# Optimization experiments

Hardware: AMD Instinct MI355X
Metric: run time of the kernel (lower is better)

## Reference

```python
import jax, jax.numpy as jnp
import numpy as np

B, M, N, D = 32, 10, 1000, 128
DEMAND_SCALER, SPEED_SCALER, PREF_SCALER = 40.0, 1.0, 1.0


def _pos_encoding(m, d, dtype):
    # standard sinusoidal PE over agent positions 0..m-1
    pos = jnp.arange(m, dtype=dtype)[:, None]
    div = jnp.exp(jnp.arange(0, d, 2, dtype=dtype) * (-jnp.log(jnp.asarray(10000.0, dtype)) / d))
    ang = pos * div  # (m, d/2)
    return jnp.stack([jnp.sin(ang), jnp.cos(ang)], axis=-1).reshape(m, d)  # even=sin, odd=cos


def setup_inputs() -> dict:
    key = jax.random.key(0)
    ks = jax.random.split(key, 14)
    return {
        "locs": jax.random.uniform(ks[0], (B, M + N, 2), jnp.float32),
        "capacity": jax.random.uniform(ks[1], (B, M), jnp.float32),
        "speed": jax.random.uniform(ks[2], (B, M), jnp.float32),
        "demand": jax.random.uniform(ks[3], (B, 1, M + N), jnp.float32),
        "agents_preference": jax.random.uniform(ks[4], (B, M, M + N), jnp.float32),
        "action_mask": jnp.ones((B, M, M + N), dtype=bool),
        "W_depot": jax.random.normal(ks[5], (D, 2), jnp.float32) * 0.1,
        "W_posproj": jax.random.normal(ks[6], (D, D), jnp.float32) * 0.05,
        "alpha": jnp.ones((1,), jnp.float32),
        "W_agents": jax.random.normal(ks[7], (D, 4), jnp.float32) * 0.1,
        "W_depot_agents": jax.random.normal(ks[8], (D, 2 * D), jnp.float32) * 0.05,
        "W_clients": jax.random.normal(ks[9], (D, 5), jnp.float32) * 0.1,
        "W_pref": jax.random.normal(ks[10], (D, 1), jnp.float32) * 0.1,
        "W_final": jax.random.normal(ks[11], (D, 3 * D), jnp.float32) * 0.05,
    }


def reference(locs, capacity, speed, demand, agents_preference, action_mask,
              W_depot, W_posproj, alpha, W_agents, W_depot_agents, W_clients,
              W_pref, W_final):
    m = action_mask.shape[-2]
    d = W_final.shape[0]
    depot_locs = locs[:, :m]            # (B, m, 2)
    agents_locs = locs[:, :m]
    clients_locs = locs[:, m:]          # (B, N, 2)

    # depot branch with positional encoding
    dep_emb = depot_locs @ W_depot.T                                   # (B, m, D)
    pe = _pos_encoding(m, d, dep_emb.dtype)                            # (m, D)
    depot_embedding = dep_emb + alpha[0] * (pe @ W_posproj.T)          # broadcast over B

    # agents branch
    agents_feats = jnp.concatenate(
        [agents_locs, capacity[..., None] / DEMAND_SCALER, speed[..., None] / SPEED_SCALER], axis=-1)
    agents_embedding = agents_feats @ W_agents.T                       # (B, m, D)
    depot_agents_embedding = jnp.concatenate(
        [depot_embedding, agents_embedding], axis=-1) @ W_depot_agents.T  # (B, m, D)

    # clients branch (with polar feats)
    demands = demand[:, 0, m:]                                         # (B, N)
    centered = clients_locs - depot_locs[:, 0:1]                       # (B, N, 2)
    dist = jnp.linalg.norm(centered, axis=-1, keepdims=True)
    angle = jnp.arctan2(centered[..., 1:], centered[..., :1])
    clients_feats = jnp.concatenate(
        [clients_locs, demands[..., None] / DEMAND_SCALER, dist, angle], axis=-1)
    clients_embedding = clients_feats @ W_clients.T                    # (B, N, D)

    nodes_embedding = jnp.concatenate([agents_embedding, clients_embedding], axis=1)  # (B, m+N, D)

    # fused final projection: Linear(3D, D) on cat([nodes, pref_embed, depot_agents])
    # == nodes @ Wn.T  +  pref_embed @ Wp.T  +  depot_agents @ Wd.T, broadcast over dims.
    # pref_embed = pref[..., None] * W_pref[:, 0]  (rank-1), so pref_embed @ Wp.T = pref[..., None] * (Wp @ W_pref[:, 0])
    Wn, Wp, Wd = W_final[:, :d], W_final[:, d:2 * d], W_final[:, 2 * d:]
    v_pref = Wp @ W_pref[:, 0]                                         # (D,)
    pref = agents_preference / PREF_SCALER                             # (B, m, m+N)
    combined_embedding = (
        (nodes_embedding @ Wn.T)[:, None, :, :]                        # (B, 1, m+N, D)
        + pref[..., None] * v_pref                                     # (B, m, m+N, D)
        + (depot_agents_embedding @ Wd.T)[:, :, None, :]               # (B, m, 1, D)
    )
    return nodes_embedding, combined_embedding
```

## Files before the change

kernel.cpp:

```cpp
#include <hip/hip_runtime.h>
#include <math.h>

#define BB 32
#define MM 10
#define NNODES 1010
#define DD 128
#define RPB 16
#define NG 64

__global__ __launch_bounds__(512) void k_front(
    const float* __restrict__ locs,
    const float* __restrict__ capacity,
    const float* __restrict__ speed,
    const float* __restrict__ W_depot,
    const float* __restrict__ W_posproj,
    const float* __restrict__ alpha,
    const float* __restrict__ W_agents,
    const float* __restrict__ W_da,
    const float* __restrict__ W_pref,
    const float* __restrict__ W_final,
    float* __restrict__ out_nodes,
    float* __restrict__ ws_daWd,
    float* __restrict__ ws_wnT,
    float* __restrict__ ws_vpref)
{
    const int bk = blockIdx.x;
    const int t = threadIdx.x;

    if (bk < BB) {
        const int b = bk;
        const int d = t >> 2;
        const int q = t & 3;

        __shared__ float pe_s[MM][DD];
        __shared__ float cat_s[2 * DD];
        __shared__ float da_s[DD];

        for (int idx = t; idx < MM * DD; idx += 512) {
            const int m = idx >> 7;
            const int k = idx & (DD - 1);
            const int i = k >> 1;
            const float div = expf((float)(2 * i) * (-logf(10000.0f) / (float)DD));
            const float ang = (float)m * div;
            pe_s[m][k] = (k & 1) ? cosf(ang) : sinf(ang);
        }

        float4 wpp[8], wfd[8], wda[16];
        {
            const float4* p = (const float4*)(W_posproj + (size_t)d * DD + q * 32);
            #pragma unroll
            for (int i = 0; i < 8; ++i) wpp[i] = p[i];
        }
        {
            const float4* p = (const float4*)(W_da + (size_t)d * 256 + q * 64);
            #pragma unroll
            for (int i = 0; i < 16; ++i) wda[i] = p[i];
        }
        {
            const float4* p = (const float4*)(W_final + (size_t)d * 384 + 256 + q * 32);
            #pragma unroll
            for (int i = 0; i < 8; ++i) wfd[i] = p[i];
        }
        const float wd0 = W_depot[d * 2 + 0], wd1 = W_depot[d * 2 + 1];
        const float wa0 = W_agents[d * 4 + 0], wa1 = W_agents[d * 4 + 1];
        const float wa2 = W_agents[d * 4 + 2], wa3 = W_agents[d * 4 + 3];
        const float al = alpha[0];
        __syncthreads();

        for (int m = 0; m < MM; ++m) {
            float pp = 0.0f;
            {
                const float4* pe4 = (const float4*)(&pe_s[m][q * 32]);
                #pragma unroll
                for (int i = 0; i < 8; ++i) {
                    const float4 w = wpp[i], x = pe4[i];
                    pp = fmaf(w.x, x.x, fmaf(w.y, x.y, fmaf(w.z, x.z, fmaf(w.w, x.w, pp))));
                }
            }
            pp += __shfl_xor(pp, 1, 4);
            pp += __shfl_xor(pp, 2, 4);

            if (q == 0) {
                const float lx = locs[((size_t)b * NNODES + m) * 2 + 0];
                const float ly = locs[((size_t)b * NNODES + m) * 2 + 1];
                const float dep = fmaf(lx, wd0, fmaf(ly, wd1, al * pp));
                const float cap = capacity[b * MM + m] * (1.0f / 40.0f);
                const float spd = speed[b * MM + m];
                const float ag = fmaf(lx, wa0, fmaf(ly, wa1,
                                 fmaf(cap, wa2, spd * wa3)));
                out_nodes[((size_t)b * NNODES + m) * DD + d] = ag;
                cat_s[d] = dep;
                cat_s[DD + d] = ag;
            }
            __syncthreads();

            float da = 0.0f;
            {
                const float4* c4 = (const float4*)(cat_s + q * 64);
                #pragma unroll
                for (int i = 0; i < 16; ++i) {
                    const float4 w = wda[i], x = c4[i];
                    da = fmaf(w.x, x.x, fmaf(w.y, x.y, fmaf(w.z, x.z, fmaf(w.w, x.w, da))));
                }
            }
            da += __shfl_xor(da, 1, 4);
            da += __shfl_xor(da, 2, 4);
            if (q == 0) da_s[d] = da;
            __syncthreads();

            float dw = 0.0f;
            {
                const float4* c4 = (const float4*)(da_s + q * 32);
                #pragma unroll
                for (int i = 0; i < 8; ++i) {
                    const float4 w = wfd[i], x = c4[i];
                    dw = fmaf(w.x, x.x, fmaf(w.y, x.y, fmaf(w.z, x.z, fmaf(w.w, x.w, dw))));
                }
            }
            dw += __shfl_xor(dw, 1, 4);
            dw += __shfl_xor(dw, 2, 4);
            if (q == 0)
                ws_daWd[(b * MM + m) * DD + d] = dw;
            __syncthreads();
        }
    } else if (bk < 48) {
        const int d = t & (DD - 1);
        const int j = t >> 7;
        const int k0 = (bk - 32) * 8;
        #pragma unroll
        for (int l = 0; l < 2; ++l) {
            const int k = k0 + j * 2 + l;
            ws_wnT[k * DD + d] = W_final[(size_t)d * 384 + k];
        }
    } else {
        if (t < DD) {
            const int d = t;
            float vp = 0.0f;
            const float4* w = (const float4*)(W_final + (size_t)d * 384 + DD);
            const float4* p = (const float4*)W_pref;
            #pragma unroll
            for (int k4 = 0; k4 < 32; ++k4) {
                const float4 a = w[k4], bb = p[k4];
                vp = fmaf(a.x, bb.x, fmaf(a.y, bb.y, fmaf(a.z, bb.z, fmaf(a.w, bb.w, vp))));
            }
            ws_vpref[d] = vp;
        }
    }
}

__global__ __launch_bounds__(256) void k_back(
    const float* __restrict__ locs,
    const float* __restrict__ demand,
    const float* __restrict__ pref,
    const float* __restrict__ W_clients,
    const float* __restrict__ wnT,
    const float* __restrict__ ws_daWd,
    const float* __restrict__ ws_vpref,
    float* __restrict__ out_nodes,
    float* __restrict__ out_comb)
{
    const int g = blockIdx.x;
    const int b = blockIdx.y;
    const int t = threadIdx.x;
    const int n0 = g * RPB;

    __shared__ float rows[RPB][DD];
    __shared__ float feat[RPB][5];
    __shared__ float pref_s[MM][RPB];

    if (t < RPB) {
        const int node = n0 + t;
        if (node < NNODES && node >= MM) {
            const float cx = locs[((size_t)b * NNODES + node) * 2 + 0];
            const float cy = locs[((size_t)b * NNODES + node) * 2 + 1];
            const float d0x = locs[((size_t)b * NNODES + 0) * 2 + 0];
            const float d0y = locs[((size_t)b * NNODES + 0) * 2 + 1];
            const float dx = cx - d0x;
            const float dy = cy - d0y;
            feat[t][0] = cx;
            feat[t][1] = cy;
            feat[t][2] = demand[(size_t)b * NNODES + node] * (1.0f / 40.0f);
            feat[t][3] = sqrtf(fmaf(dx, dx, dy * dy));
            feat[t][4] = atan2f(dy, dx);
        }
    }
    if (t < MM * RPB) {
        const int mm = t >> 4;
        const int rr = t & 15;
        const int node = n0 + rr;
        pref_s[mm][rr] = (node < NNODES)
            ? pref[(size_t)(b * MM + mm) * NNODES + node] : 0.0f;
    }
    __syncthreads();

    {
        const int d = t & (DD - 1);
        const int h = t >> 7;
        const float wc0 = W_clients[d * 5 + 0];
        const float wc1 = W_clients[d * 5 + 1];
        const float wc2 = W_clients[d * 5 + 2];
        const float wc3 = W_clients[d * 5 + 3];
        const float wc4 = W_clients[d * 5 + 4];
        #pragma unroll
        for (int i = 0; i < RPB / 2; ++i) {
            const int r = h * (RPB / 2) + i;
            const int node = n0 + r;
            float val = 0.0f;
            if (node < NNODES) {
                if (node < MM) {
                    val = out_nodes[((size_t)b * NNODES + node) * DD + d];
                } else {
                    val = fmaf(feat[r][0], wc0,
                          fmaf(feat[r][1], wc1,
                          fmaf(feat[r][2], wc2,
                          fmaf(feat[r][3], wc3,
                               feat[r][4] * wc4))));
                    out_nodes[((size_t)b * NNODES + node) * DD + d] = val;
                }
            }
            rows[r][d] = val;
        }
    }

    const int c = t & 31;
    const int s = t >> 5;
    const int col = c * 4;
    const float4 vp = *(const float4*)(ws_vpref + col);
    float4 dawd[MM];
    #pragma unroll
    for (int mm = 0; mm < MM; ++mm)
        dawd[mm] = *(const float4*)(ws_daWd + (size_t)(b * MM + mm) * DD + col);

    __syncthreads();

    float4 acc[2];
    acc[0] = make_float4(0.f, 0.f, 0.f, 0.f);
    acc[1] = make_float4(0.f, 0.f, 0.f, 0.f);
    {
        const float* wt = wnT + col;
        #pragma unroll 4
        for (int k4 = 0; k4 < DD / 4; ++k4) {
            const float4 w0 = *(const float4*)(wt + (size_t)(k4 * 4 + 0) * DD);
            const float4 w1 = *(const float4*)(wt + (size_t)(k4 * 4 + 1) * DD);
            const float4 w2 = *(const float4*)(wt + (size_t)(k4 * 4 + 2) * DD);
            const float4 w3 = *(const float4*)(wt + (size_t)(k4 * 4 + 3) * DD);
            #pragma unroll
            for (int j = 0; j < 2; ++j) {
                const float4 x = *(const float4*)&rows[s * 2 + j][k4 * 4];
                acc[j].x = fmaf(x.x, w0.x, fmaf(x.y, w1.x,
                           fmaf(x.z, w2.x, fmaf(x.w, w3.x, acc[j].x))));
                acc[j].y = fmaf(x.x, w0.y, fmaf(x.y, w1.y,
                           fmaf(x.z, w2.y, fmaf(x.w, w3.y, acc[j].y))));
                acc[j].z = fmaf(x.x, w0.z, fmaf(x.y, w1.z,
                           fmaf(x.z, w2.z, fmaf(x.w, w3.z, acc[j].z))));
                acc[j].w = fmaf(x.x, w0.w, fmaf(x.y, w1.w,
                           fmaf(x.z, w2.w, fmaf(x.w, w3.w, acc[j].w))));
            }
        }
    }

    #pragma unroll
    for (int mm = 0; mm < MM; ++mm) {
        #pragma unroll
        for (int j = 0; j < 2; ++j) {
            const int node = n0 + s * 2 + j;
            if (node >= NNODES) continue;
            const float pr = pref_s[mm][s * 2 + j];
            float4 o;
            o.x = fmaf(pr, vp.x, acc[j].x + dawd[mm].x);
            o.y = fmaf(pr, vp.y, acc[j].y + dawd[mm].y);
            o.z = fmaf(pr, vp.z, acc[j].z + dawd[mm].z);
            o.w = fmaf(pr, vp.w, acc[j].w + dawd[mm].w);
            *(float4*)(out_comb +
                ((size_t)(b * MM + mm) * NNODES + node) * DD + col) = o;
        }
    }
}

extern "C" void kernel_launch(void* const* d_in, const int* in_sizes, int n_in,
                              void* d_out, int out_size, void* d_ws, size_t ws_size,
                              hipStream_t stream) {
    const float* locs        = (const float*)d_in[0];
    const float* capacity    = (const float*)d_in[1];
    const float* speed       = (const float*)d_in[2];
    const float* demand      = (const float*)d_in[3];
    const float* agents_pref = (const float*)d_in[4];
    const float* W_depot     = (const float*)d_in[6];
    const float* W_posproj   = (const float*)d_in[7];
    const float* alpha       = (const float*)d_in[8];
    const float* W_agents    = (const float*)d_in[9];
    const float* W_da        = (const float*)d_in[10];
    const float* W_clients   = (const float*)d_in[11];
    const float* W_pref      = (const float*)d_in[12];
    const float* W_final     = (const float*)d_in[13];

    float* out_nodes = (float*)d_out;
    float* out_comb  = out_nodes + (size_t)BB * NNODES * DD;

    float* ws_daWd  = (float*)d_ws;
    float* ws_vpref = ws_daWd + BB * MM * DD;
    float* ws_wnT   = ws_vpref + DD;

    k_front<<<dim3(49), 512, 0, stream>>>(
        locs, capacity, speed, W_depot, W_posproj, alpha, W_agents,
        W_da, W_pref, W_final, out_nodes, ws_daWd, ws_wnT, ws_vpref);

    k_back<<<dim3(NG, BB), 256, 0, stream>>>(
        locs, demand, agents_pref, W_clients, ws_wnT,
        ws_daWd, ws_vpref, out_nodes, out_comb);
}
```

Measured before the change: 256.6 us.

## Split back kernel into node-projection GEMM and separate broadcast-expand kernel

```diff
diff --git a/kernel.cpp b/kernel.cpp
--- a/kernel.cpp
+++ b/kernel.cpp
@@ -5,8 +5,8 @@
 #define MM 10
 #define NNODES 1010
 #define DD 128
-#define RPB 16
-#define NG 64
+#define RPB 32
+#define NG 32
 
 __global__ __launch_bounds__(512) void k_front(
     const float* __restrict__ locs,
@@ -148,16 +148,13 @@
     }
 }
 
-__global__ __launch_bounds__(256) void k_back(
+__global__ __launch_bounds__(256) void k_nodes(
     const float* __restrict__ locs,
     const float* __restrict__ demand,
-    const float* __restrict__ pref,
     const float* __restrict__ W_clients,
     const float* __restrict__ wnT,
-    const float* __restrict__ ws_daWd,
-    const float* __restrict__ ws_vpref,
     float* __restrict__ out_nodes,
-    float* __restrict__ out_comb)
+    float* __restrict__ ws_nwn)
 {
     const int g = blockIdx.x;
     const int b = blockIdx.y;
@@ -166,7 +163,6 @@
 
     __shared__ float rows[RPB][DD];
     __shared__ float feat[RPB][5];
-    __shared__ float pref_s[MM][RPB];
 
     if (t < RPB) {
         const int node = n0 + t;
@@ -183,13 +179,6 @@
             feat[t][3] = sqrtf(fmaf(dx, dx, dy * dy));
             feat[t][4] = atan2f(dy, dx);
         }
-    }
-    if (t < MM * RPB) {
-        const int mm = t >> 4;
-        const int rr = t & 15;
-        const int node = n0 + rr;
-        pref_s[mm][rr] = (node < NNODES)
-            ? pref[(size_t)(b * MM + mm) * NNODES + node] : 0.0f;
     }
     __syncthreads();
 
@@ -221,32 +210,26 @@
             rows[r][d] = val;
         }
     }
+    __syncthreads();
 
     const int c = t & 31;
     const int s = t >> 5;
     const int col = c * 4;
-    const float4 vp = *(const float4*)(ws_vpref + col);
-    float4 dawd[MM];
+    float4 acc[4];
     #pragma unroll
-    for (int mm = 0; mm < MM; ++mm)
-        dawd[mm] = *(const float4*)(ws_daWd + (size_t)(b * MM + mm) * DD + col);
-
-    __syncthreads();
-
-    float4 acc[2];
-    acc[0] = make_float4(0.f, 0.f, 0.f, 0.f);
-    acc[1] = make_float4(0.f, 0.f, 0.f, 0.f);
+    for (int j = 0; j < 4; ++j) acc[j] = make_float4(0.f, 0.f, 0.f, 0.f);
+
     {
         const float* wt = wnT + col;
-        #pragma unroll 4
+        #pragma unroll 2
         for (int k4 = 0; k4 < DD / 4; ++k4) {
             const float4 w0 = *(const float4*)(wt + (size_t)(k4 * 4 + 0) * DD);
             const float4 w1 = *(const float4*)(wt + (size_t)(k4 * 4 + 1) * DD);
             const float4 w2 = *(const float4*)(wt + (size_t)(k4 * 4 + 2) * DD);
             const float4 w3 = *(const float4*)(wt + (size_t)(k4 * 4 + 3) * DD);
             #pragma unroll
-            for (int j = 0; j < 2; ++j) {
-                const float4 x = *(const float4*)&rows[s * 2 + j][k4 * 4];
+            for (int j = 0; j < 4; ++j) {
+                const float4 x = *(const float4*)&rows[s * 4 + j][k4 * 4];
                 acc[j].x = fmaf(x.x, w0.x, fmaf(x.y, w1.x,
                            fmaf(x.z, w2.x, fmaf(x.w, w3.x, acc[j].x))));
                 acc[j].y = fmaf(x.x, w0.y, fmaf(x.y, w1.y,
@@ -260,20 +243,43 @@
     }
 
     #pragma unroll
-    for (int mm = 0; mm < MM; ++mm) {
-        #pragma unroll
-        for (int j = 0; j < 2; ++j) {
-            const int node = n0 + s * 2 + j;
-            if (node >= NNODES) continue;
-            const float pr = pref_s[mm][s * 2 + j];
-            float4 o;
-            o.x = fmaf(pr, vp.x, acc[j].x + dawd[mm].x);
-            o.y = fmaf(pr, vp.y, acc[j].y + dawd[mm].y);
-            o.z = fmaf(pr, vp.z, acc[j].z + dawd[mm].z);
-            o.w = fmaf(pr, vp.w, acc[j].w + dawd[mm].w);
-            *(float4*)(out_comb +
-                ((size_t)(b * MM + mm) * NNODES + node) * DD + col) = o;
-        }
+    for (int j = 0; j < 4; ++j) {
+        const int node = n0 + s * 4 + j;
+        if (node < NNODES)
+            *(float4*)(ws_nwn + ((size_t)b * NNODES + node) * DD + col) = acc[j];
+    }
+}
+
+__global__ __launch_bounds__(256) void k_expand(
+    const float* __restrict__ pref,
+    const float* __restrict__ ws_nwn,
+    const float* __restrict__ ws_daWd,
+    const float* __restrict__ ws_vpref,
+    float* __restrict__ out_comb)
+{
+    const int p = blockIdx.y;
+    const int b = p / MM;
+    const int mm = p - b * MM;
+    const int t = threadIdx.x;
+    const int col = (t & 31) * 4;
+    const int n0 = blockIdx.x * 128 + (t >> 5);
+
+    const float4 vp = *(const float4*)(ws_vpref + col);
+    const float4 dw = *(const float4*)(ws_daWd + (size_t)p * DD + col);
+    const float* prf = pref + (size_t)p * NNODES;
+    const float* nwb = ws_nwn + (size_t)b * NNODES * DD;
+    float* outb = out_comb + (size_t)p * NNODES * DD;
+
+    #pragma unroll 4
+    for (int node = n0; node < min(blockIdx.x * 128 + 128, NNODES); node += 8) {
+        const float pr = prf[node];
+        const float4 nw = *(const float4*)(nwb + (size_t)node * DD + col);
+        float4 o;
+        o.x = fmaf(pr, vp.x, nw.x + dw.x);
+        o.y = fmaf(pr, vp.y, nw.y + dw.y);
+        o.z = fmaf(pr, vp.z, nw.z + dw.z);
+        o.w = fmaf(pr, vp.w, nw.w + dw.w);
+        *(float4*)(outb + (size_t)node * DD + col) = o;
     }
 }
 
@@ -300,12 +306,15 @@
     float* ws_daWd  = (float*)d_ws;
     float* ws_vpref = ws_daWd + BB * MM * DD;
     float* ws_wnT   = ws_vpref + DD;
+    float* ws_nwn   = ws_wnT + DD * DD;
 
     k_front<<<dim3(49), 512, 0, stream>>>(
         locs, capacity, speed, W_depot, W_posproj, alpha, W_agents,
         W_da, W_pref, W_final, out_nodes, ws_daWd, ws_wnT, ws_vpref);
 
-    k_back<<<dim3(NG, BB), 256, 0, stream>>>(
-        locs, demand, agents_pref, W_clients, ws_wnT,
-        ws_daWd, ws_vpref, out_nodes, out_comb);
+    k_nodes<<<dim3(NG, BB), 256, 0, stream>>>(
+        locs, demand, W_clients, ws_wnT, out_nodes, ws_nwn);
+
+    k_expand<<<dim3(8, BB * MM), 256, 0, stream>>>(
+        agents_pref, ws_nwn, ws_daWd, ws_vpref, out_comb);
 }
```

Result: slower. 273.2 us (+6.5%).
